# Optimization experiments

Hardware: AMD Instinct MI355X
Metric: run time of the kernel (lower is better)

## Reference

```python
import jax, jax.numpy as jnp
import numpy as np

H = 768      # hidden_size
NH = 12      # num_heads
HD = H // NH # head_size
MLP = 3072
B, N = 16, 577


def setup_inputs() -> dict:
    key = jax.random.key(0)
    ks = jax.random.split(key, 16)
    s = 0.02
    return {
        "x": jax.random.normal(ks[0], (B, N, H), jnp.float32),
        "Wq": jax.random.normal(ks[1], (H, H), jnp.float32) * s,
        "bq": jnp.zeros((H,), jnp.float32),
        "Wk": jax.random.normal(ks[2], (H, H), jnp.float32) * s,
        "bk": jnp.zeros((H,), jnp.float32),
        "Wv": jax.random.normal(ks[3], (H, H), jnp.float32) * s,
        "bv": jnp.zeros((H,), jnp.float32),
        "Wo": jax.random.normal(ks[4], (H, H), jnp.float32) * s,
        "bo": jnp.zeros((H,), jnp.float32),
        "W1": jax.random.normal(ks[5], (H, MLP), jnp.float32) * s,
        "b1": jnp.zeros((MLP,), jnp.float32),
        "W2": jax.random.normal(ks[6], (MLP, H), jnp.float32) * s,
        "b2": jnp.zeros((H,), jnp.float32),
        "ln1_g": jnp.ones((H,), jnp.float32),
        "ln1_b": jnp.zeros((H,), jnp.float32),
        "ln2_g": jnp.ones((H,), jnp.float32),
        "ln2_b": jnp.zeros((H,), jnp.float32),
    }


def _layernorm(x, g, b, eps=1e-6):
    mu = jnp.mean(x, axis=-1, keepdims=True)
    var = jnp.mean(jnp.square(x - mu), axis=-1, keepdims=True)
    return (x - mu) * jax.lax.rsqrt(var + eps) * g + b


def reference(x, Wq, bq, Wk, bk, Wv, bv, Wo, bo, W1, b1, W2, b2,
              ln1_g, ln1_b, ln2_g, ln2_b):
    h = x
    y = _layernorm(x, ln1_g, ln1_b)
    # projections [B,N,H] -> [B,NH,N,HD]
    def heads(t):
        return t.reshape(B, N, NH, HD).transpose(0, 2, 1, 3)
    q = heads(y @ Wq + bq)
    _k = heads(y @ Wk + bk)  # computed but UNUSED (bug in original: Q@V^T)
    v = heads(y @ Wv + bv)
    # faithful to source: scores = Q @ V^T (not K)
    scores = jnp.einsum('bhqd,bhkd->bhqk', q, v) / jnp.sqrt(jnp.float32(HD))
    probs = jax.nn.softmax(scores, axis=-1)
    o = jnp.einsum('bhqk,bhkd->bhqd', probs, v)
    o = o.transpose(0, 2, 1, 3).reshape(B, N, H)
    attn_out = o @ Wo + bo
    x1 = attn_out + h
    h2 = x1
    y2 = _layernorm(x1, ln2_g, ln2_b)
    m = jax.nn.gelu(y2 @ W1 + b1, approximate=False)
    m = m @ W2 + b2
    return m + h2
```

## Files before the change

kernel.cpp:

```cpp
#include <hip/hip_runtime.h>


#define GLOBAL_AS __attribute__((address_space(1)))
#define LDS_AS __attribute__((address_space(3)))

typedef __bf16 bf16x8 __attribute__((ext_vector_type(8)));
typedef float f32x4 __attribute__((ext_vector_type(4)));
typedef unsigned short u16x8 __attribute__((ext_vector_type(8)));

static __device__ __forceinline__ f32x4 mfma16(bf16x8 a, bf16x8 b, f32x4 c) {
  return __builtin_amdgcn_mfma_f32_16x16x32_bf16(a, b, c, 0, 0, 0);
}

static __device__ __forceinline__ unsigned short f2bf(float f) {
  union { float f; unsigned u; } v; v.f = f;
  unsigned r = v.u + 0x7fffu + ((v.u >> 16) & 1u);
  return (unsigned short)(r >> 16);
}

static __device__ __forceinline__ void async16(const void* g, void* l) {
  __builtin_amdgcn_global_load_lds((const GLOBAL_AS void*)g, (LDS_AS void*)l, 16, 0, 0);
}

static __device__ __forceinline__ float gelu_exact(float x) {
  return 0.5f * x * (1.0f + erff(x * 0.70710678118654752f));
}

static __device__ __forceinline__ void tc_body(const float* __restrict__ W,
                                               unsigned short* __restrict__ Wt,
                                               int K, int ldw, int nb, int kb,
                                               int t) {
  __shared__ float tile[32][33];
  const int tr = t >> 5, tc = t & 31;
#pragma unroll
  for (int p = 0; p < 4; ++p)
    tile[p * 8 + tr][tc] = W[(size_t)(kb + p * 8 + tr) * ldw + nb + tc];
  __syncthreads();
#pragma unroll
  for (int p = 0; p < 4; ++p)
    Wt[(size_t)(nb + p * 8 + tr) * K + kb + tc] = f2bf(tile[tc][p * 8 + tr]);
}

__global__ __launch_bounds__(256)
void transpose_cast(const float* __restrict__ W, unsigned short* __restrict__ Wt,
                    int K, int ldw) {
  tc_body(W, Wt, K, ldw, blockIdx.x * 32, blockIdx.y * 32, threadIdx.x);
}

__global__ __launch_bounds__(256)
void transpose_qv(const float* __restrict__ Wq, const float* __restrict__ Wv,
                  unsigned short* __restrict__ Wt) {
  const float* W = blockIdx.z ? Wv : Wq;
  unsigned short* dst = Wt + (size_t)blockIdx.z * 768 * 768;
  tc_body(W, dst, 768, 768, blockIdx.x * 32, blockIdx.y * 32, threadIdx.x);
}

__global__ __launch_bounds__(256)
void transpose_mlp(const float* __restrict__ W1, const float* __restrict__ W2,
                   unsigned short* __restrict__ W1Ts,
                   unsigned short* __restrict__ W2Ts, int s) {
  int id = blockIdx.x;
  if (id < 1152) {
    const int bx = id % 48, by = id / 48;
    tc_body(W1 + s * 1536, W1Ts, 768, 3072, bx * 32, by * 32, threadIdx.x);
  } else {
    id -= 1152;
    const int bx = id % 24, by = id / 24;
    tc_body(W2 + (size_t)s * 1536 * 768, W2Ts, 1536, 768, bx * 32, by * 32,
            threadIdx.x);
  }
}

__global__ __launch_bounds__(256)
void ln_f32(const float* __restrict__ x, const float* __restrict__ g,
            const float* __restrict__ be, unsigned short* __restrict__ y) {
  const int w = threadIdx.x >> 6, lane = threadIdx.x & 63;
  const size_t row = (size_t)blockIdx.x * 4 + w;
  const float* xr = x + row * 768;
  float vv[12];
#pragma unroll
  for (int j = 0; j < 3; ++j) {
    float4 v = *(const float4*)(xr + j * 256 + lane * 4);
    vv[j * 4 + 0] = v.x; vv[j * 4 + 1] = v.y;
    vv[j * 4 + 2] = v.z; vv[j * 4 + 3] = v.w;
  }
  float s = 0.f;
#pragma unroll
  for (int j = 0; j < 12; ++j) s += vv[j];
#pragma unroll
  for (int o = 32; o > 0; o >>= 1) s += __shfl_xor(s, o);
  const float mu = s * (1.0f / 768.0f);
  float q = 0.f;
#pragma unroll
  for (int j = 0; j < 12; ++j) { float d = vv[j] - mu; q += d * d; }
#pragma unroll
  for (int o = 32; o > 0; o >>= 1) q += __shfl_xor(q, o);
  const float rstd = rsqrtf(q * (1.0f / 768.0f) + 1e-6f);
  unsigned short* yr = y + row * 768;
#pragma unroll
  for (int j = 0; j < 3; ++j) {
    float4 gv = *(const float4*)(g + j * 256 + lane * 4);
    float4 bv = *(const float4*)(be + j * 256 + lane * 4);
    ushort4 o4;
    o4.x = f2bf((vv[j * 4 + 0] - mu) * rstd * gv.x + bv.x);
    o4.y = f2bf((vv[j * 4 + 1] - mu) * rstd * gv.y + bv.y);
    o4.z = f2bf((vv[j * 4 + 2] - mu) * rstd * gv.z + bv.z);
    o4.w = f2bf((vv[j * 4 + 3] - mu) * rstd * gv.w + bv.w);
    *(ushort4*)(yr + j * 256 + lane * 4) = o4;
  }
}

template <int ACT, int RES, int OUTF32, int NB, int SPLIT>
__global__ __launch_bounds__(256, 2)
void gemm_bt(const unsigned short* __restrict__ A,
             const unsigned short* __restrict__ B,
             const float* __restrict__ bias,
             const float* __restrict__ bias2,
             const float* __restrict__ resid,
             void* __restrict__ out1, void* __restrict__ out2,
             int M, int N, int K) {
  __shared__ __align__(16) unsigned short As[2][128 * 32];
  __shared__ __align__(16) unsigned short Bs[2][128 * 32];
  const int t = threadIdx.x;
  const int nwg = gridDim.x;
  const int q8 = nwg >> 3, r8 = nwg & 7;
  const int xcd = blockIdx.x & 7, jj = blockIdx.x >> 3;
  const int wgid = (xcd < r8 ? xcd * (q8 + 1) : r8 * (q8 + 1) + (xcd - r8) * q8) + jj;
  const int gn = N >> 7;
  const int m0 = (wgid / gn) * 128;
  const int n0 = (wgid % gn) * 128;
  const int w = t >> 6, lane = t & 63;
  const int lr = lane & 15, lg = lane >> 4;
  const int wrr = (w >> 1) * 64, wcc = (w & 1) * 64;
  f32x4 acc[4][4] = {};

  auto stage = [&](int buf, int k0) {
#pragma unroll
    for (int p = 0; p < 2; ++p) {
      int i = p * 256 + t;
      int row = i >> 2, c = (i & 3) << 3;
      int ar = m0 + row; ar = ar < M ? ar : M - 1;
      async16(A + (size_t)ar * K + k0 + c, &As[buf][i * 8]);
      async16(B + (size_t)(n0 + row) * K + k0 + c, &Bs[buf][i * 8]);
    }
  };

  stage(0, 0);
  int cur = 0;
  const int nt = K >> 5;
  for (int tt = 0; tt < nt; ++tt) {
    if (tt + 1 < nt) {
      stage(cur ^ 1, (tt + 1) << 5);
      asm volatile("s_waitcnt vmcnt(4)" ::: "memory");
    } else {
      asm volatile("s_waitcnt vmcnt(0)" ::: "memory");
    }
    __builtin_amdgcn_s_barrier();
    bf16x8 af[4], bfr[4];
#pragma unroll
    for (int mi = 0; mi < 4; ++mi)
      af[mi] = *(const bf16x8*)(&As[cur][(wrr + mi * 16 + lr) * 32 + lg * 8]);
#pragma unroll
    for (int ni = 0; ni < 4; ++ni)
      bfr[ni] = *(const bf16x8*)(&Bs[cur][(wcc + ni * 16 + lr) * 32 + lg * 8]);
    asm volatile("s_waitcnt lgkmcnt(0)" ::: "memory");
    __builtin_amdgcn_sched_barrier(0);
    __builtin_amdgcn_s_barrier();
#pragma unroll
    for (int mi = 0; mi < 4; ++mi)
#pragma unroll
      for (int ni = 0; ni < 4; ++ni)
        acc[mi][ni] = mfma16(af[mi], bfr[ni], acc[mi][ni]);
    cur ^= 1;
  }
  const int orow = m0 + wrr + lg * 4;
  const int ocol = n0 + wcc + lr;
#pragma unroll
  for (int mi = 0; mi < 4; ++mi) {
#pragma unroll
    for (int ni = 0; ni < 4; ++ni) {
      const int col = ocol + ni * 16;
      float bs;
      if (SPLIT)
        bs = (col < 768) ? bias[col] : bias2[col - 768];
      else
        bs = NB ? 0.f : bias[col];
      f32x4 a = acc[mi][ni];
#pragma unroll
      for (int r = 0; r < 4; ++r) {
        const int row = orow + mi * 16 + r;
        if (row < M) {
          float v = a[r] + bs;
          if (ACT == 1) v = gelu_exact(v);
          if (RES == 1) v += resid[(size_t)row * N + col];
          if (SPLIT) {
            if (col < 768)
              ((unsigned short*)out1)[(size_t)row * 768 + col] = f2bf(v);
            else
              ((unsigned short*)out2)[(size_t)row * 768 + col - 768] = f2bf(v);
          } else if (OUTF32) {
            ((float*)out1)[(size_t)row * N + col] = v;
          } else {
            ((unsigned short*)out1)[(size_t)row * N + col] = f2bf(v);
          }
        }
      }
    }
  }
}

__global__ __launch_bounds__(256, 2)
void attn_fused(const unsigned short* __restrict__ Q,
                const unsigned short* __restrict__ V,
                unsigned short* __restrict__ O) {
  __shared__ __align__(16) unsigned short Vn[64 * 72];
  __shared__ __align__(16) unsigned short Vt[64 * 72];
  __shared__ __align__(16) unsigned short Pl[4][32 * 72];
  const int qt = blockIdx.x, h = blockIdx.y, b = blockIdx.z;
  const int t = threadIdx.x, w = t >> 6, lane = t & 63;
  const int lr = lane & 15, lg = lane >> 4;
  const int q0 = qt * 128 + w * 32;
  bf16x8 aq[2][2];
#pragma unroll
  for (int mi = 0; mi < 2; ++mi) {
    int qrow = q0 + mi * 16 + lr; qrow = qrow < 577 ? qrow : 576;
    const unsigned short* qp = Q + ((size_t)(b * 577 + qrow)) * 768 + h * 64;
    aq[mi][0] = *(const bf16x8*)(qp + lg * 8);
    aq[mi][1] = *(const bf16x8*)(qp + 32 + lg * 8);
  }
  bf16x8 ones;
#pragma unroll
  for (int j = 0; j < 8; ++j) ones[j] = (__bf16)1.0f;
  f32x4 oacc[2][4] = {};
  f32x4 lac[2] = {};
  const unsigned short* vp = V + (size_t)b * 577 * 768 + h * 64;

  for (int kt = 0; kt < 10; ++kt) {
    const int k0 = kt * 64;
#pragma unroll
    for (int p = 0; p < 2; ++p) {
      int i = p * 256 + t;
      int kr = i >> 3, c = (i & 7) << 3;
      int gk = k0 + kr; gk = gk < 577 ? gk : 576;
      bf16x8 vv = *(const bf16x8*)(vp + (size_t)gk * 768 + c);
      *(bf16x8*)(Vn + kr * 72 + c) = vv;
    }
    __syncthreads();
#pragma unroll
    for (int p = 0; p < 2; ++p) {
      int i = p * 256 + t;
      int d = i & 63, kb = (i >> 6) * 8;
      u16x8 tv;
#pragma unroll
      for (int j = 0; j < 8; ++j) tv[j] = Vn[(kb + j) * 72 + d];
      *(u16x8*)(Vt + d * 72 + kb) = tv;
    }
    f32x4 s[2][4];
#pragma unroll
    for (int mi = 0; mi < 2; ++mi)
#pragma unroll
      for (int ni = 0; ni < 4; ++ni) {
        f32x4 a = {};
        a = mfma16(aq[mi][0], *(const bf16x8*)(Vn + (ni * 16 + lr) * 72 + lg * 8), a);
        a = mfma16(aq[mi][1], *(const bf16x8*)(Vn + (ni * 16 + lr) * 72 + 32 + lg * 8), a);
        s[mi][ni] = a * 0.125f;
      }
    if (kt == 9) {
#pragma unroll
      for (int ni = 0; ni < 4; ++ni) {
        int kc = k0 + ni * 16 + lr;
        if (kc >= 577) {
#pragma unroll
          for (int mi = 0; mi < 2; ++mi) {
            s[mi][ni][0] = -1e30f; s[mi][ni][1] = -1e30f;
            s[mi][ni][2] = -1e30f; s[mi][ni][3] = -1e30f;
          }
        }
      }
    }
#pragma unroll
    for (int mi = 0; mi < 2; ++mi)
#pragma unroll
      for (int ni = 0; ni < 4; ++ni)
#pragma unroll
        for (int r = 0; r < 4; ++r)
          Pl[w][(mi * 16 + lg * 4 + r) * 72 + ni * 16 + lr] =
              f2bf(__expf(s[mi][ni][r]));
    __syncthreads();
#pragma unroll
    for (int mi = 0; mi < 2; ++mi) {
      const bf16x8 pa0 = *(const bf16x8*)(&Pl[w][(mi * 16 + lr) * 72 + lg * 8]);
      const bf16x8 pa1 = *(const bf16x8*)(&Pl[w][(mi * 16 + lr) * 72 + 32 + lg * 8]);
#pragma unroll
      for (int di = 0; di < 4; ++di) {
        oacc[mi][di] = mfma16(pa0, *(const bf16x8*)(Vt + (di * 16 + lr) * 72 + lg * 8), oacc[mi][di]);
        oacc[mi][di] = mfma16(pa1, *(const bf16x8*)(Vt + (di * 16 + lr) * 72 + 32 + lg * 8), oacc[mi][di]);
      }
      lac[mi] = mfma16(pa0, ones, lac[mi]);
      lac[mi] = mfma16(pa1, ones, lac[mi]);
    }
  }
#pragma unroll
  for (int mi = 0; mi < 2; ++mi)
#pragma unroll
    for (int r = 0; r < 4; ++r) {
      const int qg = q0 + mi * 16 + lg * 4 + r;
      if (qg < 577) {
        const float inv = 1.0f / lac[mi][r];
        unsigned short* op = O + ((size_t)(b * 577 + qg)) * 768 + h * 64 + lr;
#pragma unroll
        for (int di = 0; di < 4; ++di) op[di * 16] = f2bf(oacc[mi][di][r] * inv);
      }
    }
}

extern "C" void kernel_launch(void* const* d_in, const int* in_sizes, int n_in,
                              void* d_out, int out_size, void* d_ws, size_t ws_size,
                              hipStream_t stream) {
  (void)in_sizes; (void)n_in; (void)out_size; (void)ws_size;
  const float* x   = (const float*)d_in[0];
  const float* Wq  = (const float*)d_in[1];
  const float* bq  = (const float*)d_in[2];
  const float* Wv  = (const float*)d_in[5];
  const float* bv  = (const float*)d_in[6];
  const float* Wo  = (const float*)d_in[7];
  const float* bo  = (const float*)d_in[8];
  const float* W1  = (const float*)d_in[9];
  const float* b1  = (const float*)d_in[10];
  const float* W2  = (const float*)d_in[11];
  const float* b2  = (const float*)d_in[12];
  const float* g1  = (const float*)d_in[13];
  const float* be1 = (const float*)d_in[14];
  const float* g2  = (const float*)d_in[15];
  const float* be2 = (const float*)d_in[16];
  float* out = (float*)d_out;

  const size_t BF = (size_t)9232 * 768 * 2;
  char* ws = (char*)d_ws;
  unsigned short* sA = (unsigned short*)(ws);
  unsigned short* sB = (unsigned short*)(ws + BF);
  unsigned short* sC = (unsigned short*)(ws + 2 * BF);
  unsigned short* sD = (unsigned short*)(ws + 3 * BF);
  unsigned short* mb = sC;
  const size_t WSL = (size_t)1536 * 768;

  dim3 blk(256);

  ln_f32<<<dim3(2308), blk, 0, stream>>>(x, g1, be1, sA);
  transpose_qv<<<dim3(24, 24, 2), blk, 0, stream>>>(Wq, Wv, sD);
  gemm_bt<0, 0, 0, 0, 1><<<dim3(876), blk, 0, stream>>>(
      sA, sD, bq, bv, nullptr, sB, sC, 9232, 1536, 768);

  attn_fused<<<dim3(5, 12, 16), blk, 0, stream>>>(sB, sC, sA);

  transpose_cast<<<dim3(24, 24), blk, 0, stream>>>(Wo, sD, 768, 768);
  gemm_bt<0, 1, 1, 0, 0><<<dim3(438), blk, 0, stream>>>(
      sA, sD, bo, nullptr, x, out, nullptr, 9232, 768, 768);

  ln_f32<<<dim3(2308), blk, 0, stream>>>(out, g2, be2, sB);

  transpose_mlp<<<dim3(2304), blk, 0, stream>>>(W1, W2, sA, sA + WSL, 0);
  transpose_mlp<<<dim3(2304), blk, 0, stream>>>(W1, W2, sA + 2 * WSL, sA + 3 * WSL, 1);

  for (int s = 0; s < 2; ++s) {
    unsigned short* W1Ts = sA + (size_t)(2 * s) * WSL;
    unsigned short* W2Ts = sA + (size_t)(2 * s + 1) * WSL;
    gemm_bt<1, 0, 0, 0, 0><<<dim3(876), blk, 0, stream>>>(
        sB, W1Ts, b1 + s * 1536, nullptr, nullptr, mb, nullptr, 9232, 1536, 768);
    if (s == 0) {
      gemm_bt<0, 1, 1, 0, 0><<<dim3(438), blk, 0, stream>>>(
          mb, W2Ts, b2, nullptr, out, out, nullptr, 9232, 768, 1536);
    } else {
      gemm_bt<0, 1, 1, 1, 0><<<dim3(438), blk, 0, stream>>>(
          mb, W2Ts, nullptr, nullptr, out, out, nullptr, 9232, 768, 1536);
    }
  }
}
```

Measured before the change: 347.7 us.

## Triple-buffer GEMM LDS pipeline and merge all weight transposes into one launch

The GEMM main loop moves from double to triple LDS buffering. It prefetches two K-tiles ahead, drops the second per-iteration barrier, and raises wave priority around the MFMA block. All weight transpose/cast kernels are merged into a single launch at the start, writing into a reorganized workspace layout. This is meant to hide global-load latency and cut barrier and launch overhead, at the cost of more LDS per block, which may reduce occupancy.

```diff
diff --git a/kernel.cpp b/kernel.cpp
--- a/kernel.cpp
+++ b/kernel.cpp
@@ -42,32 +42,30 @@
 }
 
 __global__ __launch_bounds__(256)
-void transpose_cast(const float* __restrict__ W, unsigned short* __restrict__ Wt,
-                    int K, int ldw) {
-  tc_body(W, Wt, K, ldw, blockIdx.x * 32, blockIdx.y * 32, threadIdx.x);
-}
-
-__global__ __launch_bounds__(256)
-void transpose_qv(const float* __restrict__ Wq, const float* __restrict__ Wv,
-                  unsigned short* __restrict__ Wt) {
-  const float* W = blockIdx.z ? Wv : Wq;
-  unsigned short* dst = Wt + (size_t)blockIdx.z * 768 * 768;
-  tc_body(W, dst, 768, 768, blockIdx.x * 32, blockIdx.y * 32, threadIdx.x);
-}
-
-__global__ __launch_bounds__(256)
-void transpose_mlp(const float* __restrict__ W1, const float* __restrict__ W2,
-                   unsigned short* __restrict__ W1Ts,
-                   unsigned short* __restrict__ W2Ts, int s) {
+void transpose_all(const float* __restrict__ Wq, const float* __restrict__ Wv,
+                   const float* __restrict__ Wo, const float* __restrict__ W1,
+                   const float* __restrict__ W2, unsigned short* __restrict__ R3) {
+  const size_t S = 589824;
   int id = blockIdx.x;
-  if (id < 1152) {
-    const int bx = id % 48, by = id / 48;
-    tc_body(W1 + s * 1536, W1Ts, 768, 3072, bx * 32, by * 32, threadIdx.x);
+  const int t = threadIdx.x;
+  if (id < 1728) {
+    const float* W = id < 576 ? Wq : (id < 1152 ? Wv : Wo);
+    unsigned short* dst = R3 + (size_t)(id / 576) * S;
+    id %= 576;
+    tc_body(W, dst, 768, 768, (id % 24) * 32, (id / 24) * 32, t);
   } else {
-    id -= 1152;
-    const int bx = id % 24, by = id / 24;
-    tc_body(W2 + (size_t)s * 1536 * 768, W2Ts, 1536, 768, bx * 32, by * 32,
-            threadIdx.x);
+    id -= 1728;
+    const int seg = id / 1152;
+    id %= 1152;
+    const int s = seg >> 1;
+    if ((seg & 1) == 0) {
+      unsigned short* dst = R3 + 3 * S + (size_t)s * 4 * S;
+      tc_body(W1 + s * 1536, dst, 768, 3072, (id % 48) * 32, (id / 48) * 32, t);
+    } else {
+      unsigned short* dst = R3 + 5 * S + (size_t)s * 4 * S;
+      tc_body(W2 + (size_t)s * 1536 * 768, dst, 1536, 768, (id % 24) * 32,
+              (id / 24) * 32, t);
+    }
   }
 }
 
@@ -119,8 +117,8 @@
              const float* __restrict__ resid,
              void* __restrict__ out1, void* __restrict__ out2,
              int M, int N, int K) {
-  __shared__ __align__(16) unsigned short As[2][128 * 32];
-  __shared__ __align__(16) unsigned short Bs[2][128 * 32];
+  __shared__ __align__(16) unsigned short As[3][128 * 32];
+  __shared__ __align__(16) unsigned short Bs[3][128 * 32];
   const int t = threadIdx.x;
   const int nwg = gridDim.x;
   const int q8 = nwg >> 3, r8 = nwg & 7;
@@ -146,16 +144,17 @@
   };
 
   stage(0, 0);
-  int cur = 0;
+  stage(1, 32);
   const int nt = K >> 5;
+  int cur = 0, nx = 2;
   for (int tt = 0; tt < nt; ++tt) {
-    if (tt + 1 < nt) {
-      stage(cur ^ 1, (tt + 1) << 5);
+    if (tt + 1 < nt)
       asm volatile("s_waitcnt vmcnt(4)" ::: "memory");
-    } else {
+    else
       asm volatile("s_waitcnt vmcnt(0)" ::: "memory");
-    }
     __builtin_amdgcn_s_barrier();
+    __builtin_amdgcn_sched_barrier(0);
+    if (tt + 2 < nt) stage(nx, (tt + 2) << 5);
     bf16x8 af[4], bfr[4];
 #pragma unroll
     for (int mi = 0; mi < 4; ++mi)
@@ -165,13 +164,15 @@
       bfr[ni] = *(const bf16x8*)(&Bs[cur][(wcc + ni * 16 + lr) * 32 + lg * 8]);
     asm volatile("s_waitcnt lgkmcnt(0)" ::: "memory");
     __builtin_amdgcn_sched_barrier(0);
-    __builtin_amdgcn_s_barrier();
+    __builtin_amdgcn_s_setprio(1);
 #pragma unroll
     for (int mi = 0; mi < 4; ++mi)
 #pragma unroll
       for (int ni = 0; ni < 4; ++ni)
         acc[mi][ni] = mfma16(af[mi], bfr[ni], acc[mi][ni]);
-    cur ^= 1;
+    __builtin_amdgcn_s_setprio(0);
+    cur = (cur == 2) ? 0 : cur + 1;
+    nx = (nx == 2) ? 0 : nx + 1;
   }
   const int orow = m0 + wrr + lg * 4;
   const int ocol = n0 + wcc + lr;
@@ -336,43 +337,42 @@
   float* out = (float*)d_out;
 
   const size_t BF = (size_t)9232 * 768 * 2;
+  const size_t S = 589824;
   char* ws = (char*)d_ws;
-  unsigned short* sA = (unsigned short*)(ws);
-  unsigned short* sB = (unsigned short*)(ws + BF);
-  unsigned short* sC = (unsigned short*)(ws + 2 * BF);
-  unsigned short* sD = (unsigned short*)(ws + 3 * BF);
-  unsigned short* mb = sC;
-  const size_t WSL = (size_t)1536 * 768;
+  unsigned short* R0 = (unsigned short*)(ws);
+  unsigned short* R1 = (unsigned short*)(ws + BF);
+  unsigned short* R2 = (unsigned short*)(ws + 2 * BF);
+  unsigned short* R3 = (unsigned short*)(ws + 3 * BF);
+  unsigned short* WqT = R3;
+  unsigned short* WoT = R3 + 2 * S;
+  unsigned short* W1T0 = R3 + 3 * S;
+  unsigned short* W2T0 = R3 + 5 * S;
+  unsigned short* W1T1 = R3 + 7 * S;
+  unsigned short* W2T1 = R3 + 9 * S;
+  unsigned short* mb = R1;
 
   dim3 blk(256);
 
-  ln_f32<<<dim3(2308), blk, 0, stream>>>(x, g1, be1, sA);
-  transpose_qv<<<dim3(24, 24, 2), blk, 0, stream>>>(Wq, Wv, sD);
+  transpose_all<<<dim3(6336), blk, 0, stream>>>(Wq, Wv, Wo, W1, W2, R3);
+
+  ln_f32<<<dim3(2308), blk, 0, stream>>>(x, g1, be1, R0);
+
   gemm_bt<0, 0, 0, 0, 1><<<dim3(876), blk, 0, stream>>>(
-      sA, sD, bq, bv, nullptr, sB, sC, 9232, 1536, 768);
-
-  attn_fused<<<dim3(5, 12, 16), blk, 0, stream>>>(sB, sC, sA);
-
-  transpose_cast<<<dim3(24, 24), blk, 0, stream>>>(Wo, sD, 768, 768);
+      R0, WqT, bq, bv, nullptr, R1, R2, 9232, 1536, 768);
+
+  attn_fused<<<dim3(5, 12, 16), blk, 0, stream>>>(R1, R2, R0);
+
   gemm_bt<0, 1, 1, 0, 0><<<dim3(438), blk, 0, stream>>>(
-      sA, sD, bo, nullptr, x, out, nullptr, 9232, 768, 768);
-
-  ln_f32<<<dim3(2308), blk, 0, stream>>>(out, g2, be2, sB);
-
-  transpose_mlp<<<dim3(2304), blk, 0, stream>>>(W1, W2, sA, sA + WSL, 0);
-  transpose_mlp<<<dim3(2304), blk, 0, stream>>>(W1, W2, sA + 2 * WSL, sA + 3 * WSL, 1);
-
-  for (int s = 0; s < 2; ++s) {
-    unsigned short* W1Ts = sA + (size_t)(2 * s) * WSL;
-    unsigned short* W2Ts = sA + (size_t)(2 * s + 1) * WSL;
-    gemm_bt<1, 0, 0, 0, 0><<<dim3(876), blk, 0, stream>>>(
-        sB, W1Ts, b1 + s * 1536, nullptr, nullptr, mb, nullptr, 9232, 1536, 768);
-    if (s == 0) {
-      gemm_bt<0, 1, 1, 0, 0><<<dim3(438), blk, 0, stream>>>(
-          mb, W2Ts, b2, nullptr, out, out, nullptr, 9232, 768, 1536);
-    } else {
-      gemm_bt<0, 1, 1, 1, 0><<<dim3(438), blk, 0, stream>>>(
-          mb, W2Ts, nullptr, nullptr, out, out, nullptr, 9232, 768, 1536);
-    }
-  }
-}
+      R0, WoT, bo, nullptr, x, out, nullptr, 9232, 768, 768);
+
+  ln_f32<<<dim3(2308), blk, 0, stream>>>(out, g2, be2, R0);
+
+  gemm_bt<1, 0, 0, 0, 0><<<dim3(876), blk, 0, stream>>>(
+      R0, W1T0, b1, nullptr, nullptr, mb, nullptr, 9232, 1536, 768);
+  gemm_bt<0, 1, 1, 0, 0><<<dim3(438), blk, 0, stream>>>(
+      mb, W2T0, b2, nullptr, out, out, nullptr, 9232, 768, 1536);
+  gemm_bt<1, 0, 0, 0, 0><<<dim3(876), blk, 0, stream>>>(
+      R0, W1T1, b1 + 1536, nullptr, nullptr, mb, nullptr, 9232, 1536, 768);
+  gemm_bt<0, 1, 1, 1, 0><<<dim3(438), blk, 0, stream>>>(
+      mb, W2T1, nullptr, nullptr, out, out, nullptr, 9232, 768, 1536);
+}
```

New measurement: 405.1 us. +16.5%, slower.
